# Kernel optimization log

Hardware: AMD Instinct MI355X
Metric: run time of the kernel (lower is better)

## Reference

```python
import jax, jax.numpy as jnp
import numpy as np

N = 50000      # num nodes
E = 800000     # num edges
D = 128        # hidden_dim
H = 2          # num_heads
A = H * D      # all_head_size


def setup_inputs() -> dict:
    key = jax.random.key(0)
    ks = jax.random.split(key, 18)
    rn = lambda k, shape, s=1.0: jax.random.normal(k, shape, jnp.float32) * s
    w = 0.05  # small init scale for weights (glorot-ish)
    return {
        "x_0": rn(ks[0], (N, D)),
        "x_1": rn(ks[1], (N, D)),
        "edge_attr": rn(ks[2], (E, D)),
        "edges": jax.random.randint(ks[3], (2, E), 0, N, jnp.int64 if jax.config.jax_enable_x64 else jnp.int32),
        "edge_types": jax.random.randint(ks[4], (E,), 0, 8, jnp.int64 if jax.config.jax_enable_x64 else jnp.int32),
        # Attention projections (stored [in, out]; equals torch Linear y = x @ W)
        "Wq": rn(ks[5], (D, A), w),   "bq": jnp.zeros((A,), jnp.float32),
        "Wk": rn(ks[6], (2 * D, A), w), "bk": jnp.zeros((A,), jnp.float32),
        "Wv": rn(ks[7], (2 * D, A), w), "bv": jnp.zeros((A,), jnp.float32),
        "Wo": rn(ks[8], (A, D), w),   "bo": jnp.zeros((D,), jnp.float32),
        # GRUCell params: gates ordered (r, z, n) as in torch
        "W_ih": rn(ks[9], (D, 3 * D), w),  "b_ih": rn(ks[10], (3 * D,), w),
        "W_hh": rn(ks[11], (D, 3 * D), w), "b_hh": rn(ks[12], (3 * D,), w),
    }


def _gru_cell(x, h, W_ih, b_ih, W_hh, b_hh):
    gi = x @ W_ih + b_ih
    gh = h @ W_hh + b_hh
    i_r, i_z, i_n = jnp.split(gi, 3, axis=-1)
    h_r, h_z, h_n = jnp.split(gh, 3, axis=-1)
    r = jax.nn.sigmoid(i_r + h_r)
    z = jax.nn.sigmoid(i_z + h_z)
    n = jnp.tanh(i_n + r * h_n)
    return (1.0 - z) * n + z * h


def reference(x_0, x_1, edge_attr, edges, edge_types,
              Wq, bq, Wk, bk, Wv, bv, Wo, bo, W_ih, b_ih, W_hh, b_hh):
    src, dst = edges[0], edges[1]            # x_j <- src, x_i <- dst
    q = (x_0[dst] @ Wq + bq).reshape(-1, H, D)            # [E,H,D]
    kv_in = jnp.concatenate([edge_attr, x_1[src]], -1)    # [E,2D]
    k = (kv_in @ Wk + bk).reshape(-1, H, D)
    v = (kv_in @ Wv + bv).reshape(-1, H, D)
    alpha = jnp.sum(q * k, -1) / jnp.sqrt(jnp.float32(D)) # [E,H]
    alpha = jax.nn.leaky_relu(alpha, 0.2)
    # segment softmax over dst (PyG softmax semantics, eps = 1e-16)
    m = jax.ops.segment_max(alpha, dst, num_segments=N)
    e = jnp.exp(alpha - m[dst])
    denom = jax.ops.segment_sum(e, dst, num_segments=N)
    a = e / (denom[dst] + 1e-16)                           # [E,H]
    aggr = jax.ops.segment_sum(a[:, :, None] * v, dst, num_segments=N)  # [N,H,D]
    msg = aggr.reshape(N, A) @ Wo + bo                     # [N,D]
    # GRUCell(input=x_0, hidden=attn_message); target_idxes = all nodes
    return _gru_cell(x_0, msg, W_ih, b_ih, W_hh, b_hh)
```

## Files before the change

### kernel.cpp

```cpp
#include <hip/hip_runtime.h>
#include <hip/hip_bf16.h>
#include <math.h>

#define NN 50000
#define EE 800000
#define MPAD 50048

#define OFF_QQBF   0ull
#define OFF_KVBF   12900000ull
#define OFF_AGGBF  25900000ull
#define OFF_MSGBF  45300000ull
#define OFF_INT    48600000ull
#define OFF_WCATQ  50500000ull
#define OFF_WCATKV 50600000ull
#define OFF_WBIG   50700000ull
#define OFF_WGRU   50800000ull
#define OFF_BCATQ  51000000ull
#define OFF_BCATKV 51001000ull
#define OFF_BGRU   51002000ull
#define OFF_PQ     51010000ull
#define OFF_PKV    51050000ull
#define OFF_PBIG   51090000ull
#define OFF_PGRU   51130000ull
#define OFF_X0BF   51200000ull

typedef short bf16x8 __attribute__((ext_vector_type(8)));
typedef float f32x4 __attribute__((ext_vector_type(4)));
typedef float fv4 __attribute__((ext_vector_type(4)));

__device__ inline unsigned short f2bf(float f) {
  unsigned u = __float_as_uint(f);
  return (unsigned short)((u + 0x7FFFu + ((u >> 16) & 1u)) >> 16);
}
__device__ inline float bf2f(unsigned short u) {
  return __uint_as_float((unsigned)u << 16);
}
__device__ inline float4 bf2f4(ushort4 u) {
  float4 r;
  r.x = bf2f(u.x); r.y = bf2f(u.y); r.z = bf2f(u.z); r.w = bf2f(u.w);
  return r;
}

__global__ void prep_all(const float* __restrict__ Wq, const float* __restrict__ bq,
                         const float* __restrict__ Wk, const float* __restrict__ bk,
                         const float* __restrict__ Wv, const float* __restrict__ bv,
                         const float* __restrict__ Wo,
                         const float* __restrict__ W_ih, const float* __restrict__ b_ih,
                         const float* __restrict__ W_hh, const float* __restrict__ b_hh,
                         float* __restrict__ WcatQ, float* __restrict__ bcatQ,
                         float* __restrict__ WcatKV, float* __restrict__ bcatKV,
                         float* __restrict__ Wbig, float* __restrict__ WgruCat,
                         float* __restrict__ bgru, int* __restrict__ zint) {
  const int bid = blockIdx.x, j = threadIdx.x;
  if (bid < 129) {
    int c0 = bid, h = j >> 7, c = j & 127;
    const float* wkrow = Wk + (size_t)c * 256 + h * 128;
    float acc = 0.f;
    if (c0 < 128) {
      const float* wqrow = Wq + (size_t)c0 * 256 + h * 128;
      for (int d = 0; d < 128; d++) acc += wqrow[d] * wkrow[d];
      WcatQ[c0 * 512 + 256 + j] = acc;
    } else {
      for (int d = 0; d < 128; d++) acc += bq[h * 128 + d] * wkrow[d];
      bcatQ[256 + j] = acc;
    }
  } else if (bid < 257) {
    int r = bid - 129;
    WcatQ[r * 512 + j] = Wq[r * 256 + j];
    WcatKV[r * 512 + j] = Wk[(size_t)(128 + r) * 256 + j];
    WcatKV[r * 512 + 256 + j] = Wv[(size_t)(128 + r) * 256 + j];
    if (r == 0) {
      bcatQ[j] = bq[j];
      bcatKV[j] = bk[j];
      bcatKV[256 + j] = bv[j];
    }
  } else if (bid < 513) {
    int r = (bid - 257) * 2 + (j >> 7), jj = j & 127;
    if (r < 256) {
      int h = r >> 7, c = r & 127;
      float acc = 0.f;
      for (int d = 0; d < 128; d++)
        acc += Wv[(size_t)c * 256 + h * 128 + d] * Wo[(size_t)(h * 128 + d) * 128 + jj];
      Wbig[r * 128 + jj] = acc;
    } else {
      Wbig[r * 128 + jj] = Wo[(size_t)(r - 256) * 128 + jj];
    }
  } else if (bid < 769) {
    int r = bid - 513;
    for (int c = j; c < 512; c += 256) {
      float v;
      if (r < 128) v = (c < 384) ? W_ih[(size_t)r * 384 + c] : 0.f;
      else {
        int rm = r - 128;
        v = (c < 256) ? W_hh[(size_t)rm * 384 + c]
                      : (c < 384 ? 0.f : W_hh[(size_t)rm * 384 + 256 + (c - 384)]);
      }
      WgruCat[(size_t)r * 512 + c] = v;
    }
  } else if (bid == 769) {
    bgru[j] = b_ih[j] + b_hh[j];
    int c1 = j + 256;
    bgru[c1] = (c1 < 384) ? b_ih[c1] : b_hh[c1 - 128];
  } else {
    int g = ((bid - 770) * 256 + j) * 4;
    if (g < 2 * NN) *reinterpret_cast<int4*>(zint + g) = make_int4(0, 0, 0, 0);
  }
}

__global__ __launch_bounds__(1024) void pack_hist(
    const float* __restrict__ WcatQ, const float* __restrict__ WcatKV,
    const float* __restrict__ Wbig, const float* __restrict__ WgruCat,
    unsigned short* __restrict__ pQ, unsigned short* __restrict__ pKV,
    unsigned short* __restrict__ pBig, unsigned short* __restrict__ pGRU,
    const int* __restrict__ edges, int* __restrict__ cnt) {
  const int bid = blockIdx.x, tid = threadIdx.x;
  if (bid < 40) {
    int idx = bid * 1024 + tid;
    const float* W; unsigned short* P; int KK, Nc;
    if (idx < 8192)       { W = WcatQ;   P = pQ;   KK = 128; Nc = 512; }
    else if (idx < 16384) { W = WcatKV;  P = pKV;  KK = 128; Nc = 512; idx -= 8192; }
    else if (idx < 24576) { W = Wbig;    P = pBig; KK = 512; Nc = 128; idx -= 16384; }
    else                  { W = WgruCat; P = pGRU; KK = 256; Nc = 512; idx -= 24576; }
    int nbs = Nc >> 4;
    int lane = idx & 63;
    int pair = idx >> 6;
    int kb = pair / nbs, nb = pair - kb * nbs;
    int kbase = kb * 32 + (lane >> 4) * 8;
    int col = nb * 16 + (lane & 15);
    unsigned short o[8];
#pragma unroll
    for (int j = 0; j < 8; ++j) o[j] = f2bf(W[(size_t)(kbase + j) * Nc + col]);
    *reinterpret_cast<bf16x8*>(P + (size_t)idx * 8) = *reinterpret_cast<bf16x8*>(o);
  } else {
    int e = (bid - 40) * 1024 + tid;
    if (e < EE) atomicAdd(&cnt[edges[EE + e]], 1);
  }
}

__global__ __launch_bounds__(1024) void scan_partial(const int* __restrict__ cnt,
                                                     int* __restrict__ basep,
                                                     int* __restrict__ bsum) {
  __shared__ int sd[1024];
  int t = threadIdx.x, g = blockIdx.x * 1024 + t;
  int v = (g < NN) ? cnt[g] : 0;
  sd[t] = v;
  __syncthreads();
  for (int d = 1; d < 1024; d <<= 1) {
    int add = (t >= d) ? sd[t - d] : 0;
    __syncthreads();
    sd[t] += add;
    __syncthreads();
  }
  if (g < NN) basep[g] = sd[t] - v;
  if (t == 1023) bsum[blockIdx.x] = sd[1023];
}

__global__ __launch_bounds__(1024) void scan_final(const int* __restrict__ bsum,
                                                   const int* __restrict__ basep,
                                                   int* __restrict__ base) {
  __shared__ int s_off;
  const int bid = blockIdx.x, tid = threadIdx.x;
  if (tid < 64) {
    int v = (tid < 49) ? bsum[tid] : 0;
    int incl = v;
#pragma unroll
    for (int off = 1; off < 64; off <<= 1) {
      int o = __shfl_up(incl, off);
      if (tid >= off) incl += o;
    }
    int ex = (bid == 0) ? 0 : __shfl(incl, bid - 1);
    if (tid == 0) s_off = ex;
  }
  __syncthreads();
  int g = bid * 1024 + tid;
  if (g < NN) base[g] = basep[g] + s_off;
  if (bid == 48 && tid == 0) base[NN] = EE;
}

template <int OUT, int AF32, int NF, int EMITA>
__device__ __forceinline__ void gemm_body(
    int bx, int by, const void* __restrict__ Av, const unsigned short* __restrict__ Wp,
    const float* __restrict__ bias, float* __restrict__ C,
    unsigned short* __restrict__ Cbf, unsigned short* __restrict__ Abf,
    int M, int Arows, int K, int Nc) {
  const int wid = threadIdx.x >> 6, lane = threadIdx.x & 63;
  const int m0 = by * 64 + wid * 16;
  const int nb0 = bx * NF;
  const int nbs = Nc >> 4;
  const int row = m0 + (lane & 15);
  const int arow = min(row, Arows - 1);
  const int kq = lane >> 4;
  f32x4 acc[NF];
#pragma unroll
  for (int nf = 0; nf < NF; ++nf) acc[nf] = 0.f;
  const int nkb = K >> 5;
  for (int kb = 0; kb < nkb; ++kb) {
    bf16x8 a;
    if (AF32) {
      const float* ap = (const float*)Av + (size_t)arow * K + kb * 32 + kq * 8;
      const float4 f0 = *(const float4*)ap;
      const float4 f1 = *(const float4*)(ap + 4);
      unsigned short t[8] = {f2bf(f0.x), f2bf(f0.y), f2bf(f0.z), f2bf(f0.w),
                             f2bf(f1.x), f2bf(f1.y), f2bf(f1.z), f2bf(f1.w)};
      a = *reinterpret_cast<bf16x8*>(t);
      if (EMITA) {
        if (bx == 0)
          *reinterpret_cast<bf16x8*>(Abf + (size_t)arow * K + kb * 32 + kq * 8) = a;
      }
    } else {
      a = *reinterpret_cast<const bf16x8*>(
          (const unsigned short*)Av + (size_t)arow * K + kb * 32 + kq * 8);
    }
#pragma unroll
    for (int nf = 0; nf < NF; ++nf) {
      bf16x8 b = *reinterpret_cast<const bf16x8*>(
          Wp + ((size_t)(kb * nbs + nb0 + nf) * 64 + lane) * 8);
      acc[nf] = __builtin_amdgcn_mfma_f32_16x16x32_bf16(a, b, acc[nf], 0, 0, 0);
    }
  }
  const int crow0 = m0 + (lane >> 4) * 4;
  const int ccol = lane & 15;
#pragma unroll
  for (int nf = 0; nf < NF; ++nf) {
    const float bv = bias[(nb0 + nf) * 16 + ccol];
#pragma unroll
    for (int r = 0; r < 4; ++r) {
      float v = acc[nf][r] + bv;
      float vp = __shfl_xor(v, 1);
      const int rr = crow0 + r;
      if (rr < M) {
        if (OUT == 2)
          C[(size_t)rr * Nc + (nb0 + nf) * 16 + ccol] = v;
        if (!(lane & 1)) {
          ushort2 o;
          o.x = f2bf(v);
          o.y = f2bf(vp);
          *reinterpret_cast<ushort2*>(Cbf + (size_t)rr * Nc +
                                      (nb0 + nf) * 16 + (ccol & ~1)) = o;
        }
      }
    }
  }
}

template <int OUT, int AF32, int NF, int EMITA>
__global__ __launch_bounds__(256) void gemm_mfma(
    const void* __restrict__ Av, const unsigned short* __restrict__ Wp,
    const float* __restrict__ bias, float* __restrict__ C,
    unsigned short* __restrict__ Cbf, unsigned short* __restrict__ Abf,
    int M, int Arows, int K, int Nc) {
  gemm_body<OUT, AF32, NF, EMITA>(blockIdx.x, blockIdx.y, Av, Wp, bias, C, Cbf,
                                  Abf, M, Arows, K, Nc);
}

__global__ __launch_bounds__(256) void scatter_proj(
    const int* __restrict__ edges, const int* __restrict__ base,
    int* __restrict__ cursor, int2* __restrict__ epairs,
    const float* __restrict__ x0, const float* __restrict__ x1,
    const unsigned short* __restrict__ pQ, const unsigned short* __restrict__ pKV,
    const float* __restrict__ bcatQ, const float* __restrict__ bcatKV,
    unsigned short* __restrict__ QQbf, unsigned short* __restrict__ KVbf,
    unsigned short* __restrict__ x0bf) {
  const int bid = blockIdx.x;
  if (bid < 3125) {
    int e = bid * 256 + threadIdx.x;
    int s = edges[e];
    int d = edges[EE + e];
    int pos = base[d] + atomicAdd(&cursor[d], 1);
    epairs[pos] = make_int2(e, s);
  } else if (bid < 6253) {
    int pb = bid - 3125;
    gemm_body<1, 1, 8, 1>(pb & 3, pb >> 2, x0, pQ, bcatQ, nullptr, QQbf, x0bf,
                          NN, NN, 128, 512);
  } else {
    int pb = bid - 6253;
    gemm_body<1, 1, 8, 0>(pb & 3, pb >> 2, x1, pKV, bcatKV, nullptr, KVbf, nullptr,
                          NN, NN, 128, 512);
  }
}

__global__ __launch_bounds__(256) void attn_wave_kernel(
    const float* __restrict__ edge_attr, const unsigned short* __restrict__ QQbf,
    const unsigned short* __restrict__ KVbf, const int* __restrict__ base,
    const int2* __restrict__ epairs, unsigned short* __restrict__ aggbf) {
  const int wid = threadIdx.x >> 6, lane = threadIdx.x & 63;
  const int n = blockIdx.x * 4 + wid;
  if (n >= NN) return;
  const int hh = lane >> 5;
  const int l = lane & 31;
  const unsigned short* qp = QQbf + (size_t)n * 512 + 4 * l;
  const float4 q0 = bf2f4(*(const ushort4*)(qp));
  const float4 q1 = bf2f4(*(const ushort4*)(qp + 128));
  const float4 w0 = bf2f4(*(const ushort4*)(qp + 256));
  const float4 w1 = bf2f4(*(const ushort4*)(qp + 384));
  const int beg = base[n], end = base[n + 1];
  float s0 = 0.f, s1 = 0.f;
  float4 ae0 = {0.f, 0.f, 0.f, 0.f}, ae1 = {0.f, 0.f, 0.f, 0.f};
  float4 av0 = {0.f, 0.f, 0.f, 0.f}, av1 = {0.f, 0.f, 0.f, 0.f};
  const float SC = 0.08838834764831845f;
  for (int p = beg; p < end; p += 2) {
    const int pe = min(p + hh, end - 1);
    const bool act = (p + hh < end);
    const int2 es = epairs[pe];
    const fv4 eav = __builtin_nontemporal_load(
        (const fv4*)(edge_attr + (size_t)es.x * 128 + 4 * l));
    const float4 ea = {eav.x, eav.y, eav.z, eav.w};
    const unsigned short* kp = KVbf + (size_t)es.y * 512 + 4 * l;
    const float4 k0 = bf2f4(*(const ushort4*)(kp));
    const float4 k1 = bf2f4(*(const ushort4*)(kp + 128));
    const float4 v0 = bf2f4(*(const ushort4*)(kp + 256));
    const float4 v1 = bf2f4(*(const ushort4*)(kp + 384));
    float p0 = ea.x * w0.x + ea.y * w0.y + ea.z * w0.z + ea.w * w0.w
             + q0.x * k0.x + q0.y * k0.y + q0.z * k0.z + q0.w * k0.w;
    float p1 = ea.x * w1.x + ea.y * w1.y + ea.z * w1.z + ea.w * w1.w
             + q1.x * k1.x + q1.y * k1.y + q1.z * k1.z + q1.w * k1.w;
#pragma unroll
    for (int off = 16; off; off >>= 1) {
      p0 += __shfl_xor(p0, off);
      p1 += __shfl_xor(p1, off);
    }
    float a0 = p0 * SC; a0 = (a0 < 0.f) ? 0.2f * a0 : a0;
    float a1 = p1 * SC; a1 = (a1 < 0.f) ? 0.2f * a1 : a1;
    const float x0 = act ? __expf(a0) : 0.f;
    const float x1 = act ? __expf(a1) : 0.f;
    s0 += x0; s1 += x1;
    ae0.x += x0 * ea.x; ae0.y += x0 * ea.y; ae0.z += x0 * ea.z; ae0.w += x0 * ea.w;
    ae1.x += x1 * ea.x; ae1.y += x1 * ea.y; ae1.z += x1 * ea.z; ae1.w += x1 * ea.w;
    av0.x += x0 * v0.x; av0.y += x0 * v0.y; av0.z += x0 * v0.z; av0.w += x0 * v0.w;
    av1.x += x1 * v1.x; av1.y += x1 * v1.y; av1.z += x1 * v1.z; av1.w += x1 * v1.w;
  }
  s0 += __shfl_xor(s0, 32); s1 += __shfl_xor(s1, 32);
  ae0.x += __shfl_xor(ae0.x, 32); ae0.y += __shfl_xor(ae0.y, 32);
  ae0.z += __shfl_xor(ae0.z, 32); ae0.w += __shfl_xor(ae0.w, 32);
  ae1.x += __shfl_xor(ae1.x, 32); ae1.y += __shfl_xor(ae1.y, 32);
  ae1.z += __shfl_xor(ae1.z, 32); ae1.w += __shfl_xor(ae1.w, 32);
  av0.x += __shfl_xor(av0.x, 32); av0.y += __shfl_xor(av0.y, 32);
  av0.z += __shfl_xor(av0.z, 32); av0.w += __shfl_xor(av0.w, 32);
  av1.x += __shfl_xor(av1.x, 32); av1.y += __shfl_xor(av1.y, 32);
  av1.z += __shfl_xor(av1.z, 32); av1.w += __shfl_xor(av1.w, 32);
  const float i0 = 1.f / (s0 + 1e-16f), i1 = 1.f / (s1 + 1e-16f);
  if (hh == 0) {
    unsigned short* op = aggbf + (size_t)n * 512 + 4 * l;
    ushort4 o;
    o.x = f2bf(ae0.x * i0); o.y = f2bf(ae0.y * i0);
    o.z = f2bf(ae0.z * i0); o.w = f2bf(ae0.w * i0);
    *(ushort4*)op = o;
    o.x = f2bf(ae1.x * i1); o.y = f2bf(ae1.y * i1);
    o.z = f2bf(ae1.z * i1); o.w = f2bf(ae1.w * i1);
    *(ushort4*)(op + 128) = o;
    o.x = f2bf(av0.x * i0); o.y = f2bf(av0.y * i0);
    o.z = f2bf(av0.z * i0); o.w = f2bf(av0.w * i0);
    *(ushort4*)(op + 256) = o;
    o.x = f2bf(av1.x * i1); o.y = f2bf(av1.y * i1);
    o.z = f2bf(av1.z * i1); o.w = f2bf(av1.w * i1);
    *(ushort4*)(op + 384) = o;
  }
}

__global__ __launch_bounds__(256) void gru_fused(
    const unsigned short* __restrict__ x0bf, const unsigned short* __restrict__ msgbf,
    const unsigned short* __restrict__ pGRU, const float* __restrict__ bgru,
    float* __restrict__ out) {
  const int wid = threadIdx.x >> 6, lane = threadIdx.x & 63;
  const int m0 = blockIdx.y * 64 + wid * 16;
  const int xq = blockIdx.x;
  const int row = m0 + (lane & 15);
  const int ar = min(row, NN - 1);
  const int kq = lane >> 4;
  f32x4 acc[4][2];
#pragma unroll
  for (int g = 0; g < 4; ++g)
#pragma unroll
    for (int f = 0; f < 2; ++f) acc[g][f] = 0.f;
  for (int kb = 0; kb < 8; ++kb) {
    bf16x8 a;
    if (kb < 4) {
      a = *reinterpret_cast<const bf16x8*>(x0bf + (size_t)ar * 128 +
                                           kb * 32 + kq * 8);
    } else {
      a = *reinterpret_cast<const bf16x8*>(msgbf + (size_t)ar * 128 +
                                           (kb - 4) * 32 + kq * 8);
    }
#pragma unroll
    for (int g = 0; g < 4; ++g)
#pragma unroll
      for (int f = 0; f < 2; ++f) {
        const int nf = g * 8 + xq * 2 + f;
        bf16x8 b = *reinterpret_cast<const bf16x8*>(
            pGRU + ((size_t)(kb * 32 + nf) * 64 + lane) * 8);
        acc[g][f] = __builtin_amdgcn_mfma_f32_16x16x32_bf16(a, b, acc[g][f], 0, 0, 0);
      }
  }
  const int crow0 = m0 + (lane >> 4) * 4;
  const int ccol = lane & 15;
#pragma unroll
  for (int f = 0; f < 2; ++f) {
    const int d = xq * 32 + f * 16 + ccol;
    const float brs = bgru[d], bzs = bgru[128 + d];
    const float bin = bgru[256 + d], bhn = bgru[384 + d];
#pragma unroll
    for (int r = 0; r < 4; ++r) {
      const int rr = crow0 + r;
      if (rr < NN) {
        const float rs = acc[0][f][r] + brs;
        const float zs = acc[1][f][r] + bzs;
        const float iv = acc[2][f][r] + bin;
        const float hv = acc[3][f][r] + bhn;
        const float rg = 1.f / (1.f + __expf(-rs));
        const float zg = 1.f / (1.f + __expf(-zs));
        const float ng = tanhf(iv + rg * hv);
        const float h = bf2f(msgbf[(size_t)rr * 128 + d]);
        out[(size_t)rr * 128 + d] = (1.f - zg) * ng + zg * h;
      }
    }
  }
}

extern "C" void kernel_launch(void* const* d_in, const int* in_sizes, int n_in,
                              void* d_out, int out_size, void* d_ws, size_t ws_size,
                              hipStream_t stream) {
  const float* x0 = (const float*)d_in[0];
  const float* x1 = (const float*)d_in[1];
  const float* edge_attr = (const float*)d_in[2];
  const int* edges = (const int*)d_in[3];
  const float* Wq = (const float*)d_in[5];
  const float* bq = (const float*)d_in[6];
  const float* Wk = (const float*)d_in[7];
  const float* bk = (const float*)d_in[8];
  const float* Wv = (const float*)d_in[9];
  const float* bv = (const float*)d_in[10];
  const float* Wo = (const float*)d_in[11];
  const float* bo = (const float*)d_in[12];
  const float* W_ih = (const float*)d_in[13];
  const float* b_ih = (const float*)d_in[14];
  const float* W_hh = (const float*)d_in[15];
  const float* b_hh = (const float*)d_in[16];
  float* out = (float*)d_out;
  float* wsf = (float*)d_ws;

  unsigned short* QQbf  = (unsigned short*)(wsf + OFF_QQBF);
  unsigned short* KVbf  = (unsigned short*)(wsf + OFF_KVBF);
  unsigned short* aggbf = (unsigned short*)(wsf + OFF_AGGBF);
  unsigned short* msgbf = (unsigned short*)(wsf + OFF_MSGBF);
  unsigned short* x0bf  = (unsigned short*)(wsf + OFF_X0BF);
  int* ip    = (int*)(wsf + OFF_INT);
  int* cntb  = ip;
  int* curb  = ip + NN;
  int* bpart = ip + 2 * NN;
  int* baseb = ip + 3 * NN;
  int* bsumb = ip + 4 * NN + 1;
  int2* epairs = (int2*)(ip + 4 * NN + 130);
  float* WcatQ  = wsf + OFF_WCATQ;
  float* WcatKV = wsf + OFF_WCATKV;
  float* Wbigb  = wsf + OFF_WBIG;
  float* WgruC  = wsf + OFF_WGRU;
  float* bcatQ  = wsf + OFF_BCATQ;
  float* bcatKV = wsf + OFF_BCATKV;
  float* bgru   = wsf + OFF_BGRU;
  unsigned short* pQ   = (unsigned short*)(wsf + OFF_PQ);
  unsigned short* pKV  = (unsigned short*)(wsf + OFF_PKV);
  unsigned short* pBig = (unsigned short*)(wsf + OFF_PBIG);
  unsigned short* pGRU = (unsigned short*)(wsf + OFF_PGRU);

  prep_all<<<870, 256, 0, stream>>>(Wq, bq, Wk, bk, Wv, bv, Wo, W_ih, b_ih,
                                    W_hh, b_hh, WcatQ, bcatQ, WcatKV, bcatKV,
                                    Wbigb, WgruC, bgru, ip);
  pack_hist<<<822, 1024, 0, stream>>>(WcatQ, WcatKV, Wbigb, WgruC,
                                      pQ, pKV, pBig, pGRU, edges, cntb);
  scan_partial<<<49, 1024, 0, stream>>>(cntb, bpart, bsumb);
  scan_final<<<49, 1024, 0, stream>>>(bsumb, bpart, baseb);
  scatter_proj<<<9381, 256, 0, stream>>>(edges, baseb, curb, epairs,
                                         x0, x1, pQ, pKV, bcatQ, bcatKV,
                                         QQbf, KVbf, x0bf);
  attn_wave_kernel<<<(NN + 3) / 4, 256, 0, stream>>>(edge_attr, QQbf, KVbf,
                                                     baseb, epairs, aggbf);
  gemm_mfma<1, 0, 4, 0><<<dim3(2, MPAD / 64), 256, 0, stream>>>(
      aggbf, pBig, bo, nullptr, msgbf, nullptr, NN, NN, 512, 128);
  gru_fused<<<dim3(4, MPAD / 64), 256, 0, stream>>>(x0bf, msgbf, pGRU, bgru, out);
}
```

Measured before the change: 441.4 us.

## Gather raw x1 instead of projected V and fold Wv into output weight

The per-node V projection of x1 is no longer computed or stored. The KV buffer now holds the K projection (256 columns) plus a bf16 copy of x1 (128 columns), giving a 384-wide row in place of 512. The attention kernel accumulates attention-weighted raw x1, and the x1 part of Wv is folded into the combined Wbig output matrix together with Wo. The bv bias is folded into a new output bias bo2, which is valid because the softmax weights sum to one. The aim is to cut the node-side GEMM work and the per-edge gather bytes in the attention kernel. In exchange, the weight prep does slightly more work.

```diff
diff --git a/kernel.cpp b/kernel.cpp
--- a/kernel.cpp
+++ b/kernel.cpp
@@ -18,6 +18,7 @@
 #define OFF_BCATQ  51000000ull
 #define OFF_BCATKV 51001000ull
 #define OFF_BGRU   51002000ull
+#define OFF_BO2    51003000ull
 #define OFF_PQ     51010000ull
 #define OFF_PKV    51050000ull
 #define OFF_PBIG   51090000ull
@@ -44,13 +45,14 @@
 __global__ void prep_all(const float* __restrict__ Wq, const float* __restrict__ bq,
                          const float* __restrict__ Wk, const float* __restrict__ bk,
                          const float* __restrict__ Wv, const float* __restrict__ bv,
-                         const float* __restrict__ Wo,
+                         const float* __restrict__ Wo, const float* __restrict__ bo,
                          const float* __restrict__ W_ih, const float* __restrict__ b_ih,
                          const float* __restrict__ W_hh, const float* __restrict__ b_hh,
                          float* __restrict__ WcatQ, float* __restrict__ bcatQ,
                          float* __restrict__ WcatKV, float* __restrict__ bcatKV,
                          float* __restrict__ Wbig, float* __restrict__ WgruCat,
-                         float* __restrict__ bgru, int* __restrict__ zint) {
+                         float* __restrict__ bgru, float* __restrict__ bo2,
+                         int* __restrict__ zint) {
   const int bid = blockIdx.x, j = threadIdx.x;
   if (bid < 129) {
     int c0 = bid, h = j >> 7, c = j & 127;
@@ -67,24 +69,19 @@
   } else if (bid < 257) {
     int r = bid - 129;
     WcatQ[r * 512 + j] = Wq[r * 256 + j];
-    WcatKV[r * 512 + j] = Wk[(size_t)(128 + r) * 256 + j];
-    WcatKV[r * 512 + 256 + j] = Wv[(size_t)(128 + r) * 256 + j];
+    if (j < 256) WcatKV[r * 256 + j] = Wk[(size_t)(128 + r) * 256 + j];
     if (r == 0) {
       bcatQ[j] = bq[j];
-      bcatKV[j] = bk[j];
-      bcatKV[256 + j] = bv[j];
+      if (j < 256) bcatKV[j] = bk[j];
     }
   } else if (bid < 513) {
     int r = (bid - 257) * 2 + (j >> 7), jj = j & 127;
-    if (r < 256) {
-      int h = r >> 7, c = r & 127;
-      float acc = 0.f;
-      for (int d = 0; d < 128; d++)
-        acc += Wv[(size_t)c * 256 + h * 128 + d] * Wo[(size_t)(h * 128 + d) * 128 + jj];
-      Wbig[r * 128 + jj] = acc;
-    } else {
-      Wbig[r * 128 + jj] = Wo[(size_t)(r - 256) * 128 + jj];
-    }
+    int h = (r >> 7) & 1, c = r & 127;
+    int srow = (r < 256) ? c : 128 + c;
+    float acc = 0.f;
+    for (int d = 0; d < 128; d++)
+      acc += Wv[(size_t)srow * 256 + h * 128 + d] * Wo[(size_t)(h * 128 + d) * 128 + jj];
+    Wbig[r * 128 + jj] = acc;
   } else if (bid < 769) {
     int r = bid - 513;
     for (int c = j; c < 512; c += 256) {
@@ -101,8 +98,14 @@
     bgru[j] = b_ih[j] + b_hh[j];
     int c1 = j + 256;
     bgru[c1] = (c1 < 384) ? b_ih[c1] : b_hh[c1 - 128];
+  } else if (bid == 770) {
+    if (j < 128) {
+      float acc = bo[j];
+      for (int t = 0; t < 256; t++) acc += bv[t] * Wo[(size_t)t * 128 + j];
+      bo2[j] = acc;
+    }
   } else {
-    int g = ((bid - 770) * 256 + j) * 4;
+    int g = ((bid - 771) * 256 + j) * 4;
     if (g < 2 * NN) *reinterpret_cast<int4*>(zint + g) = make_int4(0, 0, 0, 0);
   }
 }
@@ -114,13 +117,13 @@
     unsigned short* __restrict__ pBig, unsigned short* __restrict__ pGRU,
     const int* __restrict__ edges, int* __restrict__ cnt) {
   const int bid = blockIdx.x, tid = threadIdx.x;
-  if (bid < 40) {
+  if (bid < 36) {
     int idx = bid * 1024 + tid;
-    const float* W; unsigned short* P; int KK, Nc;
-    if (idx < 8192)       { W = WcatQ;   P = pQ;   KK = 128; Nc = 512; }
-    else if (idx < 16384) { W = WcatKV;  P = pKV;  KK = 128; Nc = 512; idx -= 8192; }
-    else if (idx < 24576) { W = Wbig;    P = pBig; KK = 512; Nc = 128; idx -= 16384; }
-    else                  { W = WgruCat; P = pGRU; KK = 256; Nc = 512; idx -= 24576; }
+    const float* W; unsigned short* P; int Nc;
+    if (idx < 8192)       { W = WcatQ;   P = pQ;   Nc = 512; }
+    else if (idx < 12288) { W = WcatKV;  P = pKV;  Nc = 256; idx -= 8192; }
+    else if (idx < 20480) { W = Wbig;    P = pBig; Nc = 128; idx -= 12288; }
+    else                  { W = WgruCat; P = pGRU; Nc = 512; idx -= 20480; }
     int nbs = Nc >> 4;
     int lane = idx & 63;
     int pair = idx >> 6;
@@ -132,7 +135,7 @@
     for (int j = 0; j < 8; ++j) o[j] = f2bf(W[(size_t)(kbase + j) * Nc + col]);
     *reinterpret_cast<bf16x8*>(P + (size_t)idx * 8) = *reinterpret_cast<bf16x8*>(o);
   } else {
-    int e = (bid - 40) * 1024 + tid;
+    int e = (bid - 36) * 1024 + tid;
     if (e < EE) atomicAdd(&cnt[edges[EE + e]], 1);
   }
 }
@@ -182,7 +185,7 @@
     int bx, int by, const void* __restrict__ Av, const unsigned short* __restrict__ Wp,
     const float* __restrict__ bias, float* __restrict__ C,
     unsigned short* __restrict__ Cbf, unsigned short* __restrict__ Abf,
-    int M, int Arows, int K, int Nc) {
+    int M, int Arows, int K, int Nc, int ldc) {
   const int wid = threadIdx.x >> 6, lane = threadIdx.x & 63;
   const int m0 = by * 64 + wid * 16;
   const int nb0 = bx * NF;
@@ -203,9 +206,13 @@
       unsigned short t[8] = {f2bf(f0.x), f2bf(f0.y), f2bf(f0.z), f2bf(f0.w),
                              f2bf(f1.x), f2bf(f1.y), f2bf(f1.z), f2bf(f1.w)};
       a = *reinterpret_cast<bf16x8*>(t);
-      if (EMITA) {
+      if (EMITA == 1) {
         if (bx == 0)
           *reinterpret_cast<bf16x8*>(Abf + (size_t)arow * K + kb * 32 + kq * 8) = a;
+      } else if (EMITA == 2) {
+        if (bx == 0)
+          *reinterpret_cast<bf16x8*>(Abf + (size_t)arow * 384 + 256 +
+                                     kb * 32 + kq * 8) = a;
       }
     } else {
       a = *reinterpret_cast<const bf16x8*>(
@@ -230,12 +237,12 @@
       const int rr = crow0 + r;
       if (rr < M) {
         if (OUT == 2)
-          C[(size_t)rr * Nc + (nb0 + nf) * 16 + ccol] = v;
+          C[(size_t)rr * ldc + (nb0 + nf) * 16 + ccol] = v;
         if (!(lane & 1)) {
           ushort2 o;
           o.x = f2bf(v);
           o.y = f2bf(vp);
-          *reinterpret_cast<ushort2*>(Cbf + (size_t)rr * Nc +
+          *reinterpret_cast<ushort2*>(Cbf + (size_t)rr * ldc +
                                       (nb0 + nf) * 16 + (ccol & ~1)) = o;
         }
       }
@@ -248,9 +255,9 @@
     const void* __restrict__ Av, const unsigned short* __restrict__ Wp,
     const float* __restrict__ bias, float* __restrict__ C,
     unsigned short* __restrict__ Cbf, unsigned short* __restrict__ Abf,
-    int M, int Arows, int K, int Nc) {
+    int M, int Arows, int K, int Nc, int ldc) {
   gemm_body<OUT, AF32, NF, EMITA>(blockIdx.x, blockIdx.y, Av, Wp, bias, C, Cbf,
-                                  Abf, M, Arows, K, Nc);
+                                  Abf, M, Arows, K, Nc, ldc);
 }
 
 __global__ __launch_bounds__(256) void scatter_proj(
@@ -271,11 +278,11 @@
   } else if (bid < 6253) {
     int pb = bid - 3125;
     gemm_body<1, 1, 8, 1>(pb & 3, pb >> 2, x0, pQ, bcatQ, nullptr, QQbf, x0bf,
-                          NN, NN, 128, 512);
+                          NN, NN, 128, 512, 512);
   } else {
     int pb = bid - 6253;
-    gemm_body<1, 1, 8, 0>(pb & 3, pb >> 2, x1, pKV, bcatKV, nullptr, KVbf, nullptr,
-                          NN, NN, 128, 512);
+    gemm_body<1, 1, 8, 2>(pb & 1, pb >> 1, x1, pKV, bcatKV, nullptr, KVbf, KVbf,
+                          NN, NN, 128, 256, 384);
   }
 }
 
@@ -305,11 +312,10 @@
     const fv4 eav = __builtin_nontemporal_load(
         (const fv4*)(edge_attr + (size_t)es.x * 128 + 4 * l));
     const float4 ea = {eav.x, eav.y, eav.z, eav.w};
-    const unsigned short* kp = KVbf + (size_t)es.y * 512 + 4 * l;
+    const unsigned short* kp = KVbf + (size_t)es.y * 384 + 4 * l;
     const float4 k0 = bf2f4(*(const ushort4*)(kp));
     const float4 k1 = bf2f4(*(const ushort4*)(kp + 128));
-    const float4 v0 = bf2f4(*(const ushort4*)(kp + 256));
-    const float4 v1 = bf2f4(*(const ushort4*)(kp + 384));
+    const float4 xb = bf2f4(*(const ushort4*)(kp + 256));
     float p0 = ea.x * w0.x + ea.y * w0.y + ea.z * w0.z + ea.w * w0.w
              + q0.x * k0.x + q0.y * k0.y + q0.z * k0.z + q0.w * k0.w;
     float p1 = ea.x * w1.x + ea.y * w1.y + ea.z * w1.z + ea.w * w1.w
@@ -326,8 +332,8 @@
     s0 += x0; s1 += x1;
     ae0.x += x0 * ea.x; ae0.y += x0 * ea.y; ae0.z += x0 * ea.z; ae0.w += x0 * ea.w;
     ae1.x += x1 * ea.x; ae1.y += x1 * ea.y; ae1.z += x1 * ea.z; ae1.w += x1 * ea.w;
-    av0.x += x0 * v0.x; av0.y += x0 * v0.y; av0.z += x0 * v0.z; av0.w += x0 * v0.w;
-    av1.x += x1 * v1.x; av1.y += x1 * v1.y; av1.z += x1 * v1.z; av1.w += x1 * v1.w;
+    av0.x += x0 * xb.x; av0.y += x0 * xb.y; av0.z += x0 * xb.z; av0.w += x0 * xb.w;
+    av1.x += x1 * xb.x; av1.y += x1 * xb.y; av1.z += x1 * xb.z; av1.w += x1 * xb.w;
   }
   s0 += __shfl_xor(s0, 32); s1 += __shfl_xor(s1, 32);
   ae0.x += __shfl_xor(ae0.x, 32); ae0.y += __shfl_xor(ae0.y, 32);
@@ -457,24 +463,25 @@
   float* bcatQ  = wsf + OFF_BCATQ;
   float* bcatKV = wsf + OFF_BCATKV;
   float* bgru   = wsf + OFF_BGRU;
+  float* bo2    = wsf + OFF_BO2;
   unsigned short* pQ   = (unsigned short*)(wsf + OFF_PQ);
   unsigned short* pKV  = (unsigned short*)(wsf + OFF_PKV);
   unsigned short* pBig = (unsigned short*)(wsf + OFF_PBIG);
   unsigned short* pGRU = (unsigned short*)(wsf + OFF_PGRU);
 
-  prep_all<<<870, 256, 0, stream>>>(Wq, bq, Wk, bk, Wv, bv, Wo, W_ih, b_ih,
+  prep_all<<<871, 256, 0, stream>>>(Wq, bq, Wk, bk, Wv, bv, Wo, bo, W_ih, b_ih,
                                     W_hh, b_hh, WcatQ, bcatQ, WcatKV, bcatKV,
-                                    Wbigb, WgruC, bgru, ip);
-  pack_hist<<<822, 1024, 0, stream>>>(WcatQ, WcatKV, Wbigb, WgruC,
+                                    Wbigb, WgruC, bgru, bo2, ip);
+  pack_hist<<<818, 1024, 0, stream>>>(WcatQ, WcatKV, Wbigb, WgruC,
                                       pQ, pKV, pBig, pGRU, edges, cntb);
   scan_partial<<<49, 1024, 0, stream>>>(cntb, bpart, bsumb);
   scan_final<<<49, 1024, 0, stream>>>(bsumb, bpart, baseb);
-  scatter_proj<<<9381, 256, 0, stream>>>(edges, baseb, curb, epairs,
+  scatter_proj<<<7817, 256, 0, stream>>>(edges, baseb, curb, epairs,
                                          x0, x1, pQ, pKV, bcatQ, bcatKV,
                                          QQbf, KVbf, x0bf);
   attn_wave_kernel<<<(NN + 3) / 4, 256, 0, stream>>>(edge_attr, QQbf, KVbf,
                                                      baseb, epairs, aggbf);
   gemm_mfma<1, 0, 4, 0><<<dim3(2, MPAD / 64), 256, 0, stream>>>(
-      aggbf, pBig, bo, nullptr, msgbf, nullptr, NN, NN, 512, 128);
+      aggbf, pBig, bo2, nullptr, msgbf, nullptr, NN, NN, 512, 128, 128);
   gru_fused<<<dim3(4, MPAD / 64), 256, 0, stream>>>(x0bf, msgbf, pGRU, bgru, out);
 }
```

Measured after the change: 397.4 us. 1.11x faster.
